# Optimization experiments

Measured on AMD Instinct MI355X. Metric: run time of the kernel, lower is better.

Reference implementation:

```python
import jax, jax.numpy as jnp
import numpy as np

D_MODEL = 1024
N_HEADS = 16
D_K = D_MODEL // N_HEADS
B, S = 2, 2048
NEG = -1000000000.0


def setup_inputs() -> dict:
    key = jax.random.key(0)
    ks = jax.random.split(key, 11)
    scale = 1.0 / np.sqrt(D_MODEL)
    inp = {
        'q': jax.random.normal(ks[0], (B, S, D_MODEL), jnp.float32),
        'k': jax.random.normal(ks[1], (B, S, D_MODEL), jnp.float32),
        'v': jax.random.normal(ks[2], (B, S, D_MODEL), jnp.float32),
        'mask': jnp.tril(jnp.ones((S, S), dtype=bool))[None, None],  # causal [1,1,S,S]
        'w_q': jax.random.normal(ks[3], (D_MODEL, D_MODEL), jnp.float32) * scale,
        'b_q': jax.random.normal(ks[4], (D_MODEL,), jnp.float32) * 0.01,
        'w_k': jax.random.normal(ks[5], (D_MODEL, D_MODEL), jnp.float32) * scale,
        'b_k': jax.random.normal(ks[6], (D_MODEL,), jnp.float32) * 0.01,
        'w_v': jax.random.normal(ks[7], (D_MODEL, D_MODEL), jnp.float32) * scale,
        'b_v': jax.random.normal(ks[8], (D_MODEL,), jnp.float32) * 0.01,
        'w_o': jax.random.normal(ks[9], (D_MODEL, D_MODEL), jnp.float32) * scale,
        'b_o': jax.random.normal(ks[10], (D_MODEL,), jnp.float32) * 0.01,
    }
    return inp


def _split_heads(x):
    b, s, _ = x.shape
    return x.reshape(b, s, N_HEADS, D_K).transpose(0, 2, 1, 3)  # [b,h,s,dk]


def reference(q, k, v, mask, w_q, b_q, w_k, b_k, w_v, b_v, w_o, b_o):
    # Linear projections (torch Linear: x @ W.T + b)
    qh = _split_heads(q @ w_q.T + b_q)
    kh = _split_heads(k @ w_k.T + b_k)
    vh = _split_heads(v @ w_v.T + b_v)
    # scaled dot-product attention (dropout is identity in eval)
    scores = jnp.einsum('bhqd,bhkd->bhqk', qh, kh) / jnp.sqrt(jnp.float32(D_K))
    scores = jnp.where(mask, scores, NEG)
    attn_weights = jax.nn.softmax(scores, axis=-1)
    out = jnp.einsum('bhqk,bhkd->bhqd', attn_weights, vh)
    out = out.transpose(0, 2, 1, 3).reshape(q.shape[0], -1, D_MODEL)
    out = out @ w_o.T + b_o
    return out, attn_weights
```

## Files before the change

kernel.cpp:

```cpp
#include <hip/hip_runtime.h>
#include <hip/hip_bf16.h>


#define DM 1024
#define NH 16
#define DKH 64
#define BB 2
#define SS 2048
#define MM (BB*SS)

typedef __bf16 bf16_t;
typedef __bf16 bf16x4 __attribute__((ext_vector_type(4)));
typedef __bf16 bf16x8 __attribute__((ext_vector_type(8)));
typedef float  f32x4  __attribute__((ext_vector_type(4)));

__device__ __forceinline__ f32x4 mfma16(bf16x8 a, bf16x8 b, f32x4 c) {
    return __builtin_amdgcn_mfma_f32_16x16x32_bf16(a, b, c, 0, 0, 0);
}
__device__ __forceinline__ bf16x8 cat8(bf16x4 lo, bf16x4 hi) {
    bf16x8 r;
    r[0]=lo[0]; r[1]=lo[1]; r[2]=lo[2]; r[3]=lo[3];
    r[4]=hi[0]; r[5]=hi[1]; r[6]=hi[2]; r[7]=hi[3];
    return r;
}

__device__ __forceinline__ void gload16(const bf16_t* g, bf16_t* l) {
    __builtin_amdgcn_global_load_lds(
        (const __attribute__((address_space(1))) void*)g,
        (__attribute__((address_space(3))) void*)l, 16, 0, 0);
}

__device__ __forceinline__ bf16x8 ldsw(const bf16_t* t, int row, int ch) {
    return *(const bf16x8*)(t + row * 64 + (((ch ^ row) & 7) << 3));
}

__global__ __launch_bounds__(256)
void cvt_bf16(const float* __restrict__ s0, const float* __restrict__ s1,
              const float* __restrict__ s2, const float* __restrict__ s3,
              bf16_t* __restrict__ d0, bf16_t* __restrict__ d1,
              bf16_t* __restrict__ d2, bf16_t* __restrict__ d3)
{
    const float* ss[4] = {s0, s1, s2, s3};
    bf16_t*      dd[4] = {d0, d1, d2, d3};
    const float* s = ss[blockIdx.y];
    bf16_t*      d = dd[blockIdx.y];
    size_t i = (size_t)(blockIdx.x * 256 + threadIdx.x) * 8;
    float4 f0 = *(const float4*)(s + i);
    float4 f1 = *(const float4*)(s + i + 4);
    bf16x8 v;
    v[0]=(bf16_t)f0.x; v[1]=(bf16_t)f0.y; v[2]=(bf16_t)f0.z; v[3]=(bf16_t)f0.w;
    v[4]=(bf16_t)f1.x; v[5]=(bf16_t)f1.y; v[6]=(bf16_t)f1.z; v[7]=(bf16_t)f1.w;
    *(bf16x8*)(d + i) = v;
}

template<int MODE>
__global__ __launch_bounds__(256)
void mha_gemm4(const bf16_t* __restrict__ A, const bf16_t* __restrict__ W,
               const float* __restrict__ bias, void* __restrict__ out)
{
    __shared__ bf16_t As[128 * 64];
    __shared__ bf16_t Bs[64 * 64];

    const int tid  = threadIdx.x;
    const int lane = tid & 63;
    const int wid  = tid >> 6;
    const int wm = wid >> 1, wn = wid & 1;
    const int bm = blockIdx.y, bn = blockIdx.x;
    const int c = lane & 15, g = lane >> 4;
    const int sr = tid >> 3, sch = tid & 7;
    const int scol = ((sch ^ (sr & 7)) << 3);

    f32x4 acc[4][2] = {};

    const bf16_t* Ab = A + (size_t)(bm * 128 + sr) * DM + scol;
    const bf16_t* Wb = W + (size_t)(bn * 64 + sr) * DM + scol;
    bf16_t* Asl = &As[(tid >> 6) * 512];
    bf16_t* Bsl = &Bs[(tid >> 6) * 512];

    for (int kt = 0; kt < DM / 64; ++kt) {
        __syncthreads();
        #pragma unroll
        for (int j = 0; j < 4; ++j)
            gload16(Ab + (size_t)(j * 32) * DM + kt * 64, Asl + j * 2048);
        #pragma unroll
        for (int j = 0; j < 2; ++j)
            gload16(Wb + (size_t)(j * 32) * DM + kt * 64, Bsl + j * 2048);
        __syncthreads();

        #pragma unroll
        for (int kh = 0; kh < 2; ++kh) {
            bf16x8 am[4], bw[2];
            #pragma unroll
            for (int f = 0; f < 4; ++f)
                am[f] = ldsw(As, wm * 64 + f * 16 + c, kh * 4 + g);
            #pragma unroll
            for (int f = 0; f < 2; ++f)
                bw[f] = ldsw(Bs, wn * 32 + f * 16 + c, kh * 4 + g);
            #pragma unroll
            for (int fm = 0; fm < 4; ++fm)
                #pragma unroll
                for (int fn = 0; fn < 2; ++fn)
                    acc[fm][fn] = mfma16(am[fm], bw[fn], acc[fm][fn]);
        }
    }

    #pragma unroll
    for (int fm = 0; fm < 4; ++fm) {
        #pragma unroll
        for (int fn = 0; fn < 2; ++fn) {
            const int col = bn * 64 + wn * 32 + fn * 16 + c;
            const float bcol = bias[col];
            if constexpr (MODE == 2) {
                const int h = (col >> 6) & 15, dk = col & 63;
                const int row0 = bm * 128 + wm * 64 + fm * 16 + 4 * g;
                const int b = row0 >> 11, s0 = row0 & (SS - 1);
                bf16x4 pv;
                #pragma unroll
                for (int r = 0; r < 4; ++r) pv[r] = (bf16_t)(acc[fm][fn][r] + bcol);
                size_t idx = ((size_t)((b * NH + h) * DKH + dk)) * SS
                           + ((s0 >> 5) << 5) + g * 8 + (fm & 1) * 4;
                *(bf16x4*)&((bf16_t*)out)[idx] = pv;
            } else {
                #pragma unroll
                for (int r = 0; r < 4; ++r) {
                    const int row = bm * 128 + wm * 64 + fm * 16 + 4 * g + r;
                    float val = acc[fm][fn][r] + bcol;
                    if constexpr (MODE == 3) {
                        ((float*)out)[(size_t)row * DM + col] = val;
                    } else {
                        if constexpr (MODE == 0) val *= 0.125f;
                        const int b = row >> 11, s = row & (SS - 1);
                        const int h = (col >> 6) & 15;
                        const int fnl = (col >> 4) & 3;
                        const int pos = ((fnl >> 1) << 5) + ((c >> 2) << 3)
                                      + ((fnl & 1) << 2) + (c & 3);
                        ((bf16_t*)out)[((size_t)(b * NH + h) * SS + s) * DKH + pos]
                            = (bf16_t)val;
                    }
                }
            }
        }
    }
}

__global__ __launch_bounds__(256)
void mha_attn4(const bf16_t* __restrict__ Qp, const bf16_t* __restrict__ Kp,
               const bf16_t* __restrict__ Vt, float* __restrict__ attn,
               bf16_t* __restrict__ aout)
{
    __shared__ bf16_t Ks[2][64 * 64];
    __shared__ bf16_t Vs[2][64 * 64];

    const int tid = threadIdx.x, lane = tid & 63, w = tid >> 6;
    const int c = lane & 15, g = lane >> 4;
    const int jb = blockIdx.x, bh = blockIdx.y;
    const int b = bh >> 4, h = bh & 15;

    const bf16_t* Qb = Qp + (size_t)bh * SS * DKH;
    const bf16_t* Kb = Kp + (size_t)bh * SS * DKH;
    const bf16_t* Vb = Vt + (size_t)bh * DKH * SS;
    float* attb = attn + (size_t)bh * SS * SS;

    const int sr = tid >> 3, sch = tid & 7;
    const int ssw = ((sch ^ (sr & 7)) << 3);

    #pragma unroll 1
    for (int half = 0; half < 2; ++half) {
        const int qt = half ? (31 - jb) : jb;
        const int q0 = qt * 64, q0w = q0 + w * 16;
        const int ntile = qt + 1;

        const bf16_t* qrow = Qb + (size_t)(q0w + c) * DKH;
        const bf16x8 qa0 = *(const bf16x8*)(qrow + g * 8);
        const bf16x8 qa1 = *(const bf16x8*)(qrow + 32 + g * 8);

        __syncthreads();
        {
            const bf16_t* src = Kb + (size_t)0 * 4096 + sr * 64 + ssw;
            gload16(src,            &Ks[0][w * 512]);
            gload16(src + 32 * 64,  &Ks[0][2048 + w * 512]);
        }
        float lsum = 0.f;
        for (int kt = 0; kt < ntile; ++kt) {
            const int cur = kt & 1;
            __syncthreads();
            if (kt + 1 < ntile) {
                const bf16_t* src = Kb + (size_t)(kt + 1) * 4096 + sr * 64 + ssw;
                gload16(src,            &Ks[cur ^ 1][w * 512]);
                gload16(src + 32 * 64,  &Ks[cur ^ 1][2048 + w * 512]);
            }
            const bf16_t* ks = Ks[cur];
            f32x4 s[4] = {};
            #pragma unroll
            for (int sub = 0; sub < 4; ++sub) {
                bf16x8 k0 = ldsw(ks, sub * 16 + c, g);
                bf16x8 k1 = ldsw(ks, sub * 16 + c, 4 | g);
                s[sub] = mfma16(k0, qa0, s[sub]);
                s[sub] = mfma16(k1, qa1, s[sub]);
            }
            if (kt == qt) {
                #pragma unroll
                for (int sub = 0; sub < 4; ++sub)
                    #pragma unroll
                    for (int r = 0; r < 4; ++r)
                        if (sub * 16 + 4 * g + r <= w * 16 + c)
                            lsum += __expf(s[sub][r]);
            } else {
                #pragma unroll
                for (int sub = 0; sub < 4; ++sub)
                    #pragma unroll
                    for (int r = 0; r < 4; ++r)
                        lsum += __expf(s[sub][r]);
            }
        }
        lsum += __shfl_xor(lsum, 16);
        lsum += __shfl_xor(lsum, 32);
        const float invl = 1.f / lsum;

        __syncthreads();
        {
            const bf16_t* ksrc = Kb + sr * 64 + ssw;
            gload16(ksrc,           &Ks[0][w * 512]);
            gload16(ksrc + 32 * 64, &Ks[0][2048 + w * 512]);
            const bf16_t* vsrc = Vb + (size_t)sr * SS + ssw;
            gload16(vsrc,                   &Vs[0][w * 512]);
            gload16(vsrc + (size_t)32 * SS, &Vs[0][2048 + w * 512]);
        }
        f32x4 o[4] = {};
        for (int kt = 0; kt < ntile; ++kt) {
            const int cur = kt & 1;
            __syncthreads();
            if (kt + 1 < ntile) {
                const bf16_t* ksrc = Kb + (size_t)(kt + 1) * 4096 + sr * 64 + ssw;
                gload16(ksrc,           &Ks[cur ^ 1][w * 512]);
                gload16(ksrc + 32 * 64, &Ks[cur ^ 1][2048 + w * 512]);
                const bf16_t* vsrc = Vb + (size_t)sr * SS + (kt + 1) * 64 + ssw;
                gload16(vsrc,                   &Vs[cur ^ 1][w * 512]);
                gload16(vsrc + (size_t)32 * SS, &Vs[cur ^ 1][2048 + w * 512]);
            }
            const bf16_t* ks = Ks[cur];
            const bf16_t* vs = Vs[cur];
            f32x4 s[4] = {};
            #pragma unroll
            for (int sub = 0; sub < 4; ++sub) {
                bf16x8 k0 = ldsw(ks, sub * 16 + c, g);
                bf16x8 k1 = ldsw(ks, sub * 16 + c, 4 | g);
                s[sub] = mfma16(k0, qa0, s[sub]);
                s[sub] = mfma16(k1, qa1, s[sub]);
            }
            const bool diag = (kt == qt);
            bf16x4 pb[4];
            float* prow = attb + (size_t)(q0w + c) * SS + kt * 64 + 4 * g;
            #pragma unroll
            for (int sub = 0; sub < 4; ++sub) {
                f32x4 pf;
                #pragma unroll
                for (int r = 0; r < 4; ++r) {
                    bool msk = diag && (sub * 16 + 4 * g + r > w * 16 + c);
                    float p = msk ? 0.f : __expf(s[sub][r]) * invl;
                    pf[r] = p;
                    pb[sub][r] = (bf16_t)p;
                }
                *(f32x4*)(prow + sub * 16) = pf;
            }
            const bf16x8 pa0 = cat8(pb[0], pb[1]);
            const bf16x8 pa1 = cat8(pb[2], pb[3]);
            #pragma unroll
            for (int fn = 0; fn < 4; ++fn) {
                bf16x8 v0 = ldsw(vs, fn * 16 + c, g);
                bf16x8 v1 = ldsw(vs, fn * 16 + c, 4 | g);
                o[fn] = mfma16(pa0, v0, o[fn]);
                o[fn] = mfma16(pa1, v1, o[fn]);
            }
        }

        #pragma unroll
        for (int fn = 0; fn < 4; ++fn)
            #pragma unroll
            for (int r = 0; r < 4; ++r)
                aout[(size_t)(b * SS + q0w + 4 * g + r) * DM + h * DKH + fn * 16 + c]
                    = (bf16_t)o[fn][r];

        {
            const int zr = q0 + (tid >> 2);
            f32x4 z = {0.f, 0.f, 0.f, 0.f};
            float* dst = attb + (size_t)zr * SS;
            for (int col = ntile * 64 + (tid & 3) * 4; col < SS; col += 16)
                *(f32x4*)(dst + col) = z;
        }
    }
}

extern "C" void kernel_launch(void* const* d_in, const int* in_sizes, int n_in,
                              void* d_out, int out_size, void* d_ws, size_t ws_size,
                              hipStream_t stream)
{
    const float* q   = (const float*)d_in[0];
    const float* k   = (const float*)d_in[1];
    const float* v   = (const float*)d_in[2];
    const float* w_q = (const float*)d_in[4];
    const float* b_q = (const float*)d_in[5];
    const float* w_k = (const float*)d_in[6];
    const float* b_k = (const float*)d_in[7];
    const float* w_v = (const float*)d_in[8];
    const float* b_v = (const float*)d_in[9];
    const float* w_o = (const float*)d_in[10];
    const float* b_o = (const float*)d_in[11];

    float* out   = (float*)d_out;
    float* attnw = out + (size_t)MM * DM;

    bf16_t* Qp   = (bf16_t*)d_ws;
    bf16_t* Kp   = Qp + (size_t)MM * DM;
    bf16_t* Vt   = Kp + (size_t)MM * DM;
    bf16_t* aout = Vt + (size_t)MM * DM;
    bf16_t* qb   = aout + (size_t)MM * DM;
    bf16_t* kb   = qb + (size_t)MM * DM;
    bf16_t* vb   = kb + (size_t)MM * DM;
    bf16_t* wqb  = vb + (size_t)MM * DM;
    bf16_t* wkb  = wqb + (size_t)DM * DM;
    bf16_t* wvb  = wkb + (size_t)DM * DM;
    bf16_t* wob  = wvb + (size_t)DM * DM;

    cvt_bf16<<<dim3(MM * DM / 2048, 3), 256, 0, stream>>>(q, k, v, q, qb, kb, vb, qb);
    cvt_bf16<<<dim3(DM * DM / 2048, 4), 256, 0, stream>>>(w_q, w_k, w_v, w_o,
                                                          wqb, wkb, wvb, wob);

    dim3 gg(DM / 64, MM / 128);
    mha_gemm4<0><<<gg, 256, 0, stream>>>(qb, wqb, b_q, Qp);
    mha_gemm4<1><<<gg, 256, 0, stream>>>(kb, wkb, b_k, Kp);
    mha_gemm4<2><<<gg, 256, 0, stream>>>(vb, wvb, b_v, Vt);

    mha_attn4<<<dim3(16, BB * NH), 256, 0, stream>>>(Qp, Kp, Vt, attnw, aout);

    mha_gemm4<3><<<gg, 256, 0, stream>>>(aout, wob, b_o, out);
}
```

Before: 276.0 us.

## Double-buffer GEMM tiles, remap blocks per XCD, merge attention halves into 512-thread blocks

The GEMMs now double-buffer their LDS tiles, dropping one barrier per k-step and prefetching the next tile while computing. Blocks are remapped from a 1D grid so each XCD handles a contiguous set of row tiles, for L2 locality. The attention kernel runs both causal halves in one 512-thread block that shares the K/V staging, folds log2(e) into the Q scale so it can use a native exp2, and uses nontemporal stores for the large attention-weight and output writes. The merged block loops over the longer half's tile count, so the waves of the shorter half sit idle at barriers, and it relies on the 8-XCD round-robin dispatch assumption.

```diff
diff --git a/kernel.cpp b/kernel.cpp
--- a/kernel.cpp
+++ b/kernel.cpp
@@ -13,6 +13,8 @@
 typedef __bf16 bf16x4 __attribute__((ext_vector_type(4)));
 typedef __bf16 bf16x8 __attribute__((ext_vector_type(8)));
 typedef float  f32x4  __attribute__((ext_vector_type(4)));
+
+#define EXP2F(x) __builtin_amdgcn_exp2f(x)
 
 __device__ __forceinline__ f32x4 mfma16(bf16x8 a, bf16x8 b, f32x4 c) {
     return __builtin_amdgcn_mfma_f32_16x16x32_bf16(a, b, c, 0, 0, 0);
@@ -55,17 +57,20 @@
 
 template<int MODE>
 __global__ __launch_bounds__(256)
-void mha_gemm4(const bf16_t* __restrict__ A, const bf16_t* __restrict__ W,
+void mha_gemm5(const bf16_t* __restrict__ A, const bf16_t* __restrict__ W,
                const float* __restrict__ bias, void* __restrict__ out)
 {
-    __shared__ bf16_t As[128 * 64];
-    __shared__ bf16_t Bs[64 * 64];
+    __shared__ bf16_t As[2][128 * 64];
+    __shared__ bf16_t Bs[2][64 * 64];
 
     const int tid  = threadIdx.x;
     const int lane = tid & 63;
     const int wid  = tid >> 6;
     const int wm = wid >> 1, wn = wid & 1;
-    const int bm = blockIdx.y, bn = blockIdx.x;
+    const int bid  = blockIdx.x;
+    const int xcd  = bid & 7, slot = bid >> 3;
+    const int bm   = xcd * 4 + (slot >> 4);
+    const int bn   = slot & 15;
     const int c = lane & 15, g = lane >> 4;
     const int sr = tid >> 3, sch = tid & 7;
     const int scol = ((sch ^ (sr & 7)) << 3);
@@ -74,28 +79,34 @@
 
     const bf16_t* Ab = A + (size_t)(bm * 128 + sr) * DM + scol;
     const bf16_t* Wb = W + (size_t)(bn * 64 + sr) * DM + scol;
-    bf16_t* Asl = &As[(tid >> 6) * 512];
-    bf16_t* Bsl = &Bs[(tid >> 6) * 512];
-
+
+#define GSTAGE(buf, kt)  do {                                              \
+        bf16_t* asl = &As[buf][wid * 512];                                 \
+        bf16_t* bsl = &Bs[buf][wid * 512];                                 \
+        _Pragma("unroll")                                                  \
+        for (int j = 0; j < 4; ++j)                                        \
+            gload16(Ab + (size_t)(j * 32) * DM + (kt) * 64, asl + j * 2048);\
+        _Pragma("unroll")                                                  \
+        for (int j = 0; j < 2; ++j)                                        \
+            gload16(Wb + (size_t)(j * 32) * DM + (kt) * 64, bsl + j * 2048);\
+    } while (0)
+
+    GSTAGE(0, 0);
     for (int kt = 0; kt < DM / 64; ++kt) {
+        const int cur = kt & 1;
         __syncthreads();
-        #pragma unroll
-        for (int j = 0; j < 4; ++j)
-            gload16(Ab + (size_t)(j * 32) * DM + kt * 64, Asl + j * 2048);
-        #pragma unroll
-        for (int j = 0; j < 2; ++j)
-            gload16(Wb + (size_t)(j * 32) * DM + kt * 64, Bsl + j * 2048);
-        __syncthreads();
-
+        if (kt + 1 < DM / 64) GSTAGE(cur ^ 1, kt + 1);
+        const bf16_t* as = As[cur];
+        const bf16_t* bs = Bs[cur];
         #pragma unroll
         for (int kh = 0; kh < 2; ++kh) {
             bf16x8 am[4], bw[2];
             #pragma unroll
             for (int f = 0; f < 4; ++f)
-                am[f] = ldsw(As, wm * 64 + f * 16 + c, kh * 4 + g);
+                am[f] = ldsw(as, wm * 64 + f * 16 + c, kh * 4 + g);
             #pragma unroll
             for (int f = 0; f < 2; ++f)
-                bw[f] = ldsw(Bs, wn * 32 + f * 16 + c, kh * 4 + g);
+                bw[f] = ldsw(bs, wn * 32 + f * 16 + c, kh * 4 + g);
             #pragma unroll
             for (int fm = 0; fm < 4; ++fm)
                 #pragma unroll
@@ -103,6 +114,7 @@
                     acc[fm][fn] = mfma16(am[fm], bw[fn], acc[fm][fn]);
         }
     }
+#undef GSTAGE
 
     #pragma unroll
     for (int fm = 0; fm < 4; ++fm) {
@@ -126,9 +138,11 @@
                     const int row = bm * 128 + wm * 64 + fm * 16 + 4 * g + r;
                     float val = acc[fm][fn][r] + bcol;
                     if constexpr (MODE == 3) {
-                        ((float*)out)[(size_t)row * DM + col] = val;
+                        __builtin_nontemporal_store(
+                            val, &((float*)out)[(size_t)row * DM + col]);
                     } else {
-                        if constexpr (MODE == 0) val *= 0.125f;
+                        if constexpr (MODE == 0)
+                            val *= 0.125f * 1.44269504f;
                         const int b = row >> 11, s = row & (SS - 1);
                         const int h = (col >> 6) & 15;
                         const int fnl = (col >> 4) & 3;
@@ -143,8 +157,8 @@
     }
 }
 
-__global__ __launch_bounds__(256)
-void mha_attn4(const bf16_t* __restrict__ Qp, const bf16_t* __restrict__ Kp,
+__global__ __launch_bounds__(512, 4)
+void mha_attn5(const bf16_t* __restrict__ Qp, const bf16_t* __restrict__ Kp,
                const bf16_t* __restrict__ Vt, float* __restrict__ attn,
                bf16_t* __restrict__ aout)
 {
@@ -153,7 +167,15 @@
 
     const int tid = threadIdx.x, lane = tid & 63, w = tid >> 6;
     const int c = lane & 15, g = lane >> 4;
-    const int jb = blockIdx.x, bh = blockIdx.y;
+    const int bid = blockIdx.x;
+    const int xcd = bid & 7, slot = bid >> 3;
+    const int bh  = ((slot & 3) << 3) | xcd;
+    const int j   = slot >> 2;
+    const int sub = w >> 2, wl = w & 3;
+    const int qt  = sub ? (31 - j) : j;
+    const int q0  = qt * 64, q0w = q0 + wl * 16;
+    const int NT  = 32 - j;
+    const int myNT = qt + 1;
     const int b = bh >> 4, h = bh & 15;
 
     const bf16_t* Qb = Qp + (size_t)bh * SS * DKH;
@@ -164,104 +186,86 @@
     const int sr = tid >> 3, sch = tid & 7;
     const int ssw = ((sch ^ (sr & 7)) << 3);
 
-    #pragma unroll 1
-    for (int half = 0; half < 2; ++half) {
-        const int qt = half ? (31 - jb) : jb;
-        const int q0 = qt * 64, q0w = q0 + w * 16;
-        const int ntile = qt + 1;
-
-        const bf16_t* qrow = Qb + (size_t)(q0w + c) * DKH;
-        const bf16x8 qa0 = *(const bf16x8*)(qrow + g * 8);
-        const bf16x8 qa1 = *(const bf16x8*)(qrow + 32 + g * 8);
-
+    const bf16_t* qrow = Qb + (size_t)(q0w + c) * DKH;
+    const bf16x8 qa0 = *(const bf16x8*)(qrow + g * 8);
+    const bf16x8 qa1 = *(const bf16x8*)(qrow + 32 + g * 8);
+
+    gload16(Kb + sr * 64 + ssw, &Ks[0][w * 512]);
+    float lsum = 0.f;
+    for (int kt = 0; kt < NT; ++kt) {
+        const int cur = kt & 1;
         __syncthreads();
-        {
-            const bf16_t* src = Kb + (size_t)0 * 4096 + sr * 64 + ssw;
-            gload16(src,            &Ks[0][w * 512]);
-            gload16(src + 32 * 64,  &Ks[0][2048 + w * 512]);
-        }
-        float lsum = 0.f;
-        for (int kt = 0; kt < ntile; ++kt) {
-            const int cur = kt & 1;
-            __syncthreads();
-            if (kt + 1 < ntile) {
-                const bf16_t* src = Kb + (size_t)(kt + 1) * 4096 + sr * 64 + ssw;
-                gload16(src,            &Ks[cur ^ 1][w * 512]);
-                gload16(src + 32 * 64,  &Ks[cur ^ 1][2048 + w * 512]);
-            }
+        if (kt + 1 < NT)
+            gload16(Kb + (size_t)(kt + 1) * 4096 + sr * 64 + ssw,
+                    &Ks[cur ^ 1][w * 512]);
+        if (kt < myNT) {
             const bf16_t* ks = Ks[cur];
             f32x4 s[4] = {};
             #pragma unroll
-            for (int sub = 0; sub < 4; ++sub) {
-                bf16x8 k0 = ldsw(ks, sub * 16 + c, g);
-                bf16x8 k1 = ldsw(ks, sub * 16 + c, 4 | g);
-                s[sub] = mfma16(k0, qa0, s[sub]);
-                s[sub] = mfma16(k1, qa1, s[sub]);
+            for (int sb = 0; sb < 4; ++sb) {
+                bf16x8 k0 = ldsw(ks, sb * 16 + c, g);
+                bf16x8 k1 = ldsw(ks, sb * 16 + c, 4 | g);
+                s[sb] = mfma16(k0, qa0, s[sb]);
+                s[sb] = mfma16(k1, qa1, s[sb]);
             }
             if (kt == qt) {
                 #pragma unroll
-                for (int sub = 0; sub < 4; ++sub)
+                for (int sb = 0; sb < 4; ++sb)
                     #pragma unroll
                     for (int r = 0; r < 4; ++r)
-                        if (sub * 16 + 4 * g + r <= w * 16 + c)
-                            lsum += __expf(s[sub][r]);
+                        if (sb * 16 + 4 * g + r <= wl * 16 + c)
+                            lsum += EXP2F(s[sb][r]);
             } else {
                 #pragma unroll
-                for (int sub = 0; sub < 4; ++sub)
+                for (int sb = 0; sb < 4; ++sb)
                     #pragma unroll
                     for (int r = 0; r < 4; ++r)
-                        lsum += __expf(s[sub][r]);
-            }
-        }
-        lsum += __shfl_xor(lsum, 16);
-        lsum += __shfl_xor(lsum, 32);
-        const float invl = 1.f / lsum;
-
+                        lsum += EXP2F(s[sb][r]);
+            }
+        }
+    }
+    lsum += __shfl_xor(lsum, 16);
+    lsum += __shfl_xor(lsum, 32);
+    const float invl = 1.f / lsum;
+
+    __syncthreads();
+    gload16(Kb + sr * 64 + ssw, &Ks[0][w * 512]);
+    gload16(Vb + (size_t)sr * SS + ssw, &Vs[0][w * 512]);
+    f32x4 o[4] = {};
+    for (int kt = 0; kt < NT; ++kt) {
+        const int cur = kt & 1;
         __syncthreads();
-        {
-            const bf16_t* ksrc = Kb + sr * 64 + ssw;
-            gload16(ksrc,           &Ks[0][w * 512]);
-            gload16(ksrc + 32 * 64, &Ks[0][2048 + w * 512]);
-            const bf16_t* vsrc = Vb + (size_t)sr * SS + ssw;
-            gload16(vsrc,                   &Vs[0][w * 512]);
-            gload16(vsrc + (size_t)32 * SS, &Vs[0][2048 + w * 512]);
-        }
-        f32x4 o[4] = {};
-        for (int kt = 0; kt < ntile; ++kt) {
-            const int cur = kt & 1;
-            __syncthreads();
-            if (kt + 1 < ntile) {
-                const bf16_t* ksrc = Kb + (size_t)(kt + 1) * 4096 + sr * 64 + ssw;
-                gload16(ksrc,           &Ks[cur ^ 1][w * 512]);
-                gload16(ksrc + 32 * 64, &Ks[cur ^ 1][2048 + w * 512]);
-                const bf16_t* vsrc = Vb + (size_t)sr * SS + (kt + 1) * 64 + ssw;
-                gload16(vsrc,                   &Vs[cur ^ 1][w * 512]);
-                gload16(vsrc + (size_t)32 * SS, &Vs[cur ^ 1][2048 + w * 512]);
-            }
+        if (kt + 1 < NT) {
+            gload16(Kb + (size_t)(kt + 1) * 4096 + sr * 64 + ssw,
+                    &Ks[cur ^ 1][w * 512]);
+            gload16(Vb + (size_t)sr * SS + (kt + 1) * 64 + ssw,
+                    &Vs[cur ^ 1][w * 512]);
+        }
+        if (kt < myNT) {
             const bf16_t* ks = Ks[cur];
             const bf16_t* vs = Vs[cur];
             f32x4 s[4] = {};
             #pragma unroll
-            for (int sub = 0; sub < 4; ++sub) {
-                bf16x8 k0 = ldsw(ks, sub * 16 + c, g);
-                bf16x8 k1 = ldsw(ks, sub * 16 + c, 4 | g);
-                s[sub] = mfma16(k0, qa0, s[sub]);
-                s[sub] = mfma16(k1, qa1, s[sub]);
+            for (int sb = 0; sb < 4; ++sb) {
+                bf16x8 k0 = ldsw(ks, sb * 16 + c, g);
+                bf16x8 k1 = ldsw(ks, sb * 16 + c, 4 | g);
+                s[sb] = mfma16(k0, qa0, s[sb]);
+                s[sb] = mfma16(k1, qa1, s[sb]);
             }
             const bool diag = (kt == qt);
             bf16x4 pb[4];
             float* prow = attb + (size_t)(q0w + c) * SS + kt * 64 + 4 * g;
             #pragma unroll
-            for (int sub = 0; sub < 4; ++sub) {
+            for (int sb = 0; sb < 4; ++sb) {
                 f32x4 pf;
                 #pragma unroll
                 for (int r = 0; r < 4; ++r) {
-                    bool msk = diag && (sub * 16 + 4 * g + r > w * 16 + c);
-                    float p = msk ? 0.f : __expf(s[sub][r]) * invl;
+                    bool msk = diag && (sb * 16 + 4 * g + r > wl * 16 + c);
+                    float p = msk ? 0.f : EXP2F(s[sb][r]) * invl;
                     pf[r] = p;
-                    pb[sub][r] = (bf16_t)p;
+                    pb[sb][r] = (bf16_t)p;
                 }
-                *(f32x4*)(prow + sub * 16) = pf;
+                __builtin_nontemporal_store(pf, (f32x4*)(prow + sb * 16));
             }
             const bf16x8 pa0 = cat8(pb[0], pb[1]);
             const bf16x8 pa1 = cat8(pb[2], pb[3]);
@@ -273,21 +277,22 @@
                 o[fn] = mfma16(pa1, v1, o[fn]);
             }
         }
-
+    }
+
+    #pragma unroll
+    for (int fn = 0; fn < 4; ++fn)
         #pragma unroll
-        for (int fn = 0; fn < 4; ++fn)
-            #pragma unroll
-            for (int r = 0; r < 4; ++r)
-                aout[(size_t)(b * SS + q0w + 4 * g + r) * DM + h * DKH + fn * 16 + c]
-                    = (bf16_t)o[fn][r];
-
-        {
-            const int zr = q0 + (tid >> 2);
-            f32x4 z = {0.f, 0.f, 0.f, 0.f};
-            float* dst = attb + (size_t)zr * SS;
-            for (int col = ntile * 64 + (tid & 3) * 4; col < SS; col += 16)
-                *(f32x4*)(dst + col) = z;
-        }
+        for (int r = 0; r < 4; ++r)
+            aout[(size_t)(b * SS + q0w + 4 * g + r) * DM + h * DKH + fn * 16 + c]
+                = (bf16_t)o[fn][r];
+
+    {
+        const int stid = tid & 255;
+        const int zr = q0 + (stid >> 2);
+        f32x4 z = {0.f, 0.f, 0.f, 0.f};
+        float* dst = attb + (size_t)zr * SS;
+        for (int col = myNT * 64 + (stid & 3) * 4; col < SS; col += 16)
+            __builtin_nontemporal_store(z, (f32x4*)(dst + col));
     }
 }
 
@@ -326,12 +331,11 @@
     cvt_bf16<<<dim3(DM * DM / 2048, 4), 256, 0, stream>>>(w_q, w_k, w_v, w_o,
                                                           wqb, wkb, wvb, wob);
 
-    dim3 gg(DM / 64, MM / 128);
-    mha_gemm4<0><<<gg, 256, 0, stream>>>(qb, wqb, b_q, Qp);
-    mha_gemm4<1><<<gg, 256, 0, stream>>>(kb, wkb, b_k, Kp);
-    mha_gemm4<2><<<gg, 256, 0, stream>>>(vb, wvb, b_v, Vt);
-
-    mha_attn4<<<dim3(16, BB * NH), 256, 0, stream>>>(Qp, Kp, Vt, attnw, aout);
-
-    mha_gemm4<3><<<gg, 256, 0, stream>>>(aout, wob, b_o, out);
-}
+    mha_gemm5<0><<<512, 256, 0, stream>>>(qb, wqb, b_q, Qp);
+    mha_gemm5<1><<<512, 256, 0, stream>>>(kb, wkb, b_k, Kp);
+    mha_gemm5<2><<<512, 256, 0, stream>>>(vb, wvb, b_v, Vt);
+
+    mha_attn5<<<512, 512, 0, stream>>>(Qp, Kp, Vt, attnw, aout);
+
+    mha_gemm5<3><<<512, 256, 0, stream>>>(aout, wob, b_o, out);
+}
```

New measurement: 307.9 us. +11.5%, slower.
